# Optimization experiments

Hardware: AMD Instinct MI355X
Metric: run time of the kernel (lower is better)

The kernel has to match this reference:

```python
import jax, jax.numpy as jnp
import numpy as np

B, N, E, H = 64, 512, 1024, 16
DH = E // H


def setup_inputs() -> dict:
    key = jax.random.key(0)
    ks = jax.random.split(key, 5)
    x = jax.random.normal(ks[0], (B, N, E), dtype=jnp.float32)
    # Linear weights stored as [in, out] (transpose of torch's [out, in]); y = x @ W + b
    Wqkv = jax.random.normal(ks[1], (E, 3 * E), dtype=jnp.float32) * 0.02
    bqkv = jnp.zeros((3 * E,), dtype=jnp.float32)
    Wproj = jax.random.normal(ks[2], (E, E), dtype=jnp.float32) * 0.02
    bproj = jnp.zeros((E,), dtype=jnp.float32)
    adj = jax.random.randint(ks[3], (N, N), 0, 2, dtype=jnp.int32)
    return {"x": x, "Wqkv": Wqkv, "bqkv": bqkv, "Wproj": Wproj, "bproj": bproj, "adj": adj}


def reference(x, Wqkv, bqkv, Wproj, bproj, adj):
    b, n, e = x.shape
    h, dh = H, e // H
    # fused QKV projection
    qkv = (x @ Wqkv + bqkv).reshape(b, n, 3, h, dh)
    qkv = jnp.transpose(qkv, (2, 0, 3, 1, 4))  # [3, B, H, N, Dh]
    q, k, v = qkv[0], qkv[1], qkv[2]
    # adjacency mask with self-loops (adj + eye, then bool), broadcast over B, H
    mask = (adj + jnp.eye(n, dtype=adj.dtype)) > 0  # [N, N]
    scale = 1.0 / jnp.sqrt(jnp.asarray(dh, dtype=x.dtype))
    scores = jnp.einsum("bhnd,bhmd->bhnm", q, k) * scale  # [B, H, N, N]
    scores = jnp.where(mask[None, None], scores, jnp.finfo(scores.dtype).min)
    attn = jax.nn.softmax(scores, axis=-1)
    y = jnp.einsum("bhnm,bhmd->bhnd", attn, v)  # [B, H, N, Dh]
    y = jnp.transpose(y, (0, 2, 1, 3)).reshape(b, n, e)
    return y @ Wproj + bproj
```

## Files before the change

### kernel.cpp

```cpp
#include <hip/hip_runtime.h>
#include <hip/hip_bf16.h>

#define Bz 64
#define Nz 512
#define Ez 1024
#define Hz 16
#define DHz 64

static constexpr int MROWS = Bz * Nz;
static constexpr int NQKV  = 3 * Ez;

typedef __attribute__((ext_vector_type(8))) short bf16x8_t;
typedef __attribute__((ext_vector_type(4))) float f32x4_t;
typedef __attribute__((ext_vector_type(16))) float f32x16_t;
typedef __attribute__((ext_vector_type(4))) unsigned u32x4_t;

union FragU { bf16x8_t h; u32x4_t u; };

__device__ __forceinline__ unsigned short f2bf(float f) {
    union { float f; unsigned u; } v; v.f = f;
    unsigned r = v.u + 0x7FFFu + ((v.u >> 16) & 1u);
    return (unsigned short)(r >> 16);
}
__device__ __forceinline__ float bf2f(unsigned short h) {
    union { unsigned u; float f; } v; v.u = ((unsigned)h) << 16;
    return v.f;
}
__device__ __forceinline__ unsigned packbf(float a, float b) {
    union { float f; unsigned u; } x, y; x.f = a; y.f = b;
    return ((x.u + 0x8000u) >> 16) | ((y.u + 0x8000u) & 0xFFFF0000u);
}

__device__ __forceinline__ void async16(const unsigned short* g, unsigned short* l) {
    __builtin_amdgcn_global_load_lds(
        (const __attribute__((address_space(1))) void*)g,
        (__attribute__((address_space(3))) void*)l, 16, 0, 0);
}

__global__ void cvt_f32_bf16(const float* __restrict__ in,
                             unsigned short* __restrict__ out, int n4) {
    int id = blockIdx.x * blockDim.x + threadIdx.x;
    int stride = gridDim.x * blockDim.x;
    for (int i = id; i < n4; i += stride) {
        float4 f = ((const float4*)in)[i];
        ushort4 o;
        o.x = f2bf(f.x); o.y = f2bf(f.y); o.z = f2bf(f.z); o.w = f2bf(f.w);
        ((ushort4*)out)[i] = o;
    }
}

__global__ __launch_bounds__(256)
void cvt_transpose(const float* __restrict__ in,
                   unsigned short* __restrict__ out,
                   int K, int Ncols) {
    int n  = blockIdx.x * 256 + threadIdx.x;
    int k0 = blockIdx.y * 8;
    bf16x8_t o;
#pragma unroll
    for (int j = 0; j < 8; j++)
        o[j] = (short)f2bf(in[(long)(k0 + j) * Ncols + n]);
    *(bf16x8_t*)&out[(long)n * K + k0] = o;
}

__global__ void build_adjm(const int* __restrict__ adj,
                           unsigned long long* __restrict__ adjm) {
    int id = blockIdx.x * blockDim.x + threadIdx.x;
    int n = id >> 3, w = id & 7;
    const int4* r4 = (const int4*)(adj + (long)n * Nz + w * 64);
    unsigned long long m = 0;
#pragma unroll
    for (int c = 0; c < 16; c++) {
        int4 v = r4[c];
        unsigned long long bits =
            (unsigned long long)(v.x != 0) | ((unsigned long long)(v.y != 0) << 1) |
            ((unsigned long long)(v.z != 0) << 2) | ((unsigned long long)(v.w != 0) << 3);
        m |= bits << (c * 4);
    }
    if ((n >> 6) == w) m |= 1ull << (n & 63);
    adjm[id] = m;
}

template<bool OUT_BF16>
__global__ __launch_bounds__(256)
void gemm_mfma(const unsigned short* __restrict__ A,
               const unsigned short* __restrict__ BT,
               const float* __restrict__ bias,
               void* __restrict__ C,
               int M, int Ncols, int K) {
    const int tid  = threadIdx.x;
    const int wave = tid >> 6;
    const int lane = tid & 63;
    const int wm = (wave >> 1) * 64;
    const int wn = (wave & 1) * 64;
    const int m32 = lane & 31;
    const int kh  = lane >> 5;

    const int rowBase = blockIdx.y * 128;
    const int colBase = blockIdx.x * 128;

    __shared__ __align__(16) unsigned short As[128][64];
    __shared__ __align__(16) unsigned short Bs[128][64];

    f32x16_t acc[2][2];
#pragma unroll
    for (int i = 0; i < 2; i++)
#pragma unroll
        for (int j = 0; j < 2; j++)
#pragma unroll
            for (int r = 0; r < 16; r++)
                acc[i][j][r] = 0.0f;

    const unsigned short* pa[4];
    const unsigned short* pb[4];
#pragma unroll
    for (int cc = 0; cc < 4; cc++) {
        int s = tid + cc * 256;
        int r = s >> 3;
        int c = (s & 7) ^ (r & 7);
        pa[cc] = &A [(long)(rowBase + r) * K + c * 8];
        pb[cc] = &BT[(long)(colBase + r) * K + c * 8];
    }
    const int fsw = m32 & 7;

    for (int k0 = 0; k0 < K; k0 += 64) {
        __syncthreads();
#pragma unroll
        for (int cc = 0; cc < 4; cc++) {
            async16(pa[cc] + k0, (unsigned short*)As + (size_t)(cc * 64 + wave * 16) * 32);
            async16(pb[cc] + k0, (unsigned short*)Bs + (size_t)(cc * 64 + wave * 16) * 32);
        }
        __syncthreads();

        bf16x8_t af[2][4], bfr[2][4];
#pragma unroll
        for (int kc = 0; kc < 4; kc++) {
            int p = (kc * 2 + kh) ^ fsw;
#pragma unroll
            for (int t = 0; t < 2; t++) {
                af[t][kc]  = *(bf16x8_t*)&As[wm + t * 32 + m32][p * 8];
                bfr[t][kc] = *(bf16x8_t*)&Bs[wn + t * 32 + m32][p * 8];
            }
        }
#pragma unroll
        for (int kc = 0; kc < 4; kc++)
#pragma unroll
            for (int i = 0; i < 2; i++)
#pragma unroll
                for (int j = 0; j < 2; j++)
                    acc[i][j] = __builtin_amdgcn_mfma_f32_32x32x16_bf16(
                        af[i][kc], bfr[j][kc], acc[i][j], 0, 0, 0);
    }

#pragma unroll
    for (int j = 0; j < 2; j++) {
        int col = colBase + wn + j * 32 + m32;
        float bv = bias[col];
#pragma unroll
        for (int i = 0; i < 2; i++) {
#pragma unroll
            for (int reg = 0; reg < 16; reg++) {
                int row = rowBase + wm + i * 32 + (reg & 3) + 8 * (reg >> 2) + 4 * kh;
                float v = acc[i][j][reg] + bv;
                if (OUT_BF16)
                    ((unsigned short*)C)[(long)row * Ncols + col] = f2bf(v);
                else
                    ((float*)C)[(long)row * Ncols + col] = v;
            }
        }
    }
}

__global__ __launch_bounds__(512, 2)
void attn_mfma(const unsigned short* __restrict__ qkv,
               const unsigned long long* __restrict__ adjm,
               unsigned short* __restrict__ y)
{
    const int h = blockIdx.x;
    const int b = blockIdx.y;
    const int tid  = threadIdx.x;
    const int lane = tid & 63;
    const int w    = tid >> 6;
    const int l16  = lane & 15;
    const int q    = lane >> 4;

    __shared__ __align__(16) unsigned short Ks[512][64];
    __shared__ __align__(16) unsigned short Vt[64][512];

    const long rowB = (long)b * Nz;
    const unsigned short* base = qkv + rowB * NQKV;

    for (int idx = tid; idx < 4096; idx += 512) {
        int n = idx >> 3, cc = idx & 7;
        *(bf16x8_t*)&Ks[n][(cc ^ (n & 7)) * 8] =
            *(const bf16x8_t*)&base[(long)n * NQKV + Ez + h * DHz + cc * 8];
    }
    {
        int tp = tid & 255, dh = tid >> 8;
        int n0 = tp * 2;
        bf16x8_t va[4], vb[4];
#pragma unroll
        for (int c = 0; c < 4; c++) {
            va[c] = *(const bf16x8_t*)&base[(long)n0 * NQKV + 2 * Ez + h * DHz + dh * 32 + c * 8];
            vb[c] = *(const bf16x8_t*)&base[(long)(n0 + 1) * NQKV + 2 * Ez + h * DHz + dh * 32 + c * 8];
        }
        unsigned short* vt = &Vt[0][0];
#pragma unroll
        for (int dd = 0; dd < 32; dd++) {
            int d = dh * 32 + dd;
            unsigned lo = (unsigned)(unsigned short)va[dd >> 3][dd & 7];
            unsigned hi = (unsigned)(unsigned short)vb[dd >> 3][dd & 7];
            int cp = (n0 >> 3) ^ (d & 7);
            *(unsigned*)&vt[d * 512 + cp * 8 + (n0 & 7)] = lo | (hi << 16);
        }
    }
    FragU qf[4][2];
#pragma unroll
    for (int mt = 0; mt < 4; mt++)
#pragma unroll
        for (int kc = 0; kc < 2; kc++)
            qf[mt][kc].h = *(const bf16x8_t*)&base[(long)(w * 64 + mt * 16 + l16) * NQKV
                                                   + h * DHz + kc * 32 + q * 8];
    __syncthreads();

    f32x4_t oacc[4][4];
#pragma unroll
    for (int mt = 0; mt < 4; mt++)
#pragma unroll
        for (int dt = 0; dt < 4; dt++) {
            f32x4_t z = {0.0f, 0.0f, 0.0f, 0.0f};
            oacc[mt][dt] = z;
        }
    float rsum[4] = {0.0f, 0.0f, 0.0f, 0.0f};
    unsigned long long wm[4];

    for (int ct = 0; ct < 16; ct++) {
        const int j0 = ct * 32;
        if ((ct & 1) == 0) {
#pragma unroll
            for (int mt = 0; mt < 4; mt++)
                wm[mt] = adjm[(size_t)(w * 64 + mt * 16 + l16) * 8 + (ct >> 1)];
        }
        bf16x8_t kf[2][2];
#pragma unroll
        for (int jt = 0; jt < 2; jt++)
#pragma unroll
            for (int kc = 0; kc < 2; kc++)
                kf[jt][kc] = *(const bf16x8_t*)
                    &Ks[j0 + jt * 16 + l16][((kc * 4 + q) ^ (l16 & 7)) * 8];

        f32x4_t tacc[2][4];
#pragma unroll
        for (int jt = 0; jt < 2; jt++)
#pragma unroll
            for (int mt = 0; mt < 4; mt++) {
                f32x4_t z = {0.0f, 0.0f, 0.0f, 0.0f};
                z = __builtin_amdgcn_mfma_f32_16x16x32_bf16(kf[jt][0], qf[mt][0].h, z, 0, 0, 0);
                tacc[jt][mt] = __builtin_amdgcn_mfma_f32_16x16x32_bf16(kf[jt][1], qf[mt][1].h, z, 0, 0, 0);
            }

        unsigned pk[2][4][2];
#pragma unroll
        for (int jt = 0; jt < 2; jt++)
#pragma unroll
            for (int mt = 0; mt < 4; mt++) {
                float e[4];
#pragma unroll
                for (int r = 0; r < 4; r++) {
                    int jrel = (ct & 1) * 32 + jt * 16 + q * 4 + r;
                    bool bit = (wm[mt] >> jrel) & 1ull;
                    float ev = bit ? __expf(tacc[jt][mt][r] * 0.125f) : 0.0f;
                    e[r] = ev;
                    rsum[mt] += ev;
                }
                pk[jt][mt][0] = packbf(e[0], e[1]);
                pk[jt][mt][1] = packbf(e[2], e[3]);
            }

        bf16x8_t vf[4];
#pragma unroll
        for (int dt = 0; dt < 4; dt++) {
            int d = dt * 16 + l16;
            int cp = (ct * 4 + q) ^ (l16 & 7);
            vf[dt] = *(const bf16x8_t*)&(&Vt[0][0])[d * 512 + cp * 8];
        }

#pragma unroll
        for (int mt = 0; mt < 4; mt++) {
            FragU pf;
#pragma unroll
            for (int p = 0; p < 4; p++) {
                int srcl = ((lane & 16) << 1) | ((p & 2) << 3) | l16;
                unsigned a0 = (unsigned)__shfl((int)pk[0][mt][p & 1], srcl);
                unsigned a1 = (unsigned)__shfl((int)pk[1][mt][p & 1], srcl);
                pf.u[p] = (lane & 32) ? a1 : a0;
            }
#pragma unroll
            for (int dt = 0; dt < 4; dt++)
                oacc[mt][dt] = __builtin_amdgcn_mfma_f32_16x16x32_bf16(
                    pf.h, vf[dt], oacc[mt][dt], 0, 0, 0);
        }
    }

#pragma unroll
    for (int mt = 0; mt < 4; mt++) {
        float s = rsum[mt];
        s += __shfl_xor(s, 16);
        s += __shfl_xor(s, 32);
#pragma unroll
        for (int r = 0; r < 4; r++) {
            float rs = __shfl(s, (lane & 48) | (q * 4) | r);
            float inv = 1.0f / rs;
            int row = w * 64 + mt * 16 + q * 4 + r;
#pragma unroll
            for (int dt = 0; dt < 4; dt++)
                y[(rowB + row) * Ez + h * DHz + dt * 16 + l16] =
                    f2bf(oacc[mt][dt][r] * inv);
        }
    }
}

extern "C" void kernel_launch(void* const* d_in, const int* in_sizes, int n_in,
                              void* d_out, int out_size, void* d_ws, size_t ws_size,
                              hipStream_t stream) {
    const float* x     = (const float*)d_in[0];
    const float* Wqkv  = (const float*)d_in[1];
    const float* bqkv  = (const float*)d_in[2];
    const float* Wproj = (const float*)d_in[3];
    const float* bproj = (const float*)d_in[4];
    const int*   adj   = (const int*)d_in[5];
    float* out = (float*)d_out;

    char* ws = (char*)d_ws;
    unsigned short* xb     = (unsigned short*)(ws);
    unsigned short* qkv    = (unsigned short*)(ws + 67108864);
    unsigned short* WqkvT  = (unsigned short*)(ws + 268435456);
    unsigned short* WprojT = (unsigned short*)(ws + 274726912);
    unsigned long long* adjm = (unsigned long long*)(ws + 276824064);
    unsigned short* yb = xb;

    cvt_f32_bf16<<<8192, 256, 0, stream>>>(x, xb, (Bz * Nz * Ez) / 4);
    cvt_transpose<<<dim3(NQKV / 256, Ez / 8), 256, 0, stream>>>(Wqkv, WqkvT, Ez, NQKV);
    cvt_transpose<<<dim3(Ez / 256, Ez / 8), 256, 0, stream>>>(Wproj, WprojT, Ez, Ez);
    build_adjm<<<16, 256, 0, stream>>>(adj, adjm);

    gemm_mfma<true><<<dim3(NQKV / 128, MROWS / 128), 256, 0, stream>>>(
        xb, WqkvT, bqkv, qkv, MROWS, NQKV, Ez);

    attn_mfma<<<dim3(Hz, Bz), 512, 0, stream>>>(qkv, adjm, yb);

    gemm_mfma<false><<<dim3(Ez / 128, MROWS / 128), 256, 0, stream>>>(
        yb, WprojT, bproj, out, MROWS, Ez, Ez);
}
```

Baseline: 744.0 us.

## Restructure GEMM to 256x256 tiles with double-buffered async LDS pipeline

The bf16 MFMA GEMM goes from 128x128 tiles with 4 waves to 256x256 tiles with 8 waves. Global-to-LDS async loads for A and B are double-buffered and staggered across two half-phases per k-step, so loads overlap MFMA work and synchronisation is reduced. It also adds an XCD-aware block-index swizzle and raises wave priority around MFMA bursts. In exchange it uses four times the LDS (128KB) and more accumulator registers, which limits occupancy and adds fragile vmcnt-based synchronisation.

```diff
diff --git a/kernel.cpp b/kernel.cpp
--- a/kernel.cpp
+++ b/kernel.cpp
@@ -35,6 +35,13 @@
     __builtin_amdgcn_global_load_lds(
         (const __attribute__((address_space(1))) void*)g,
         (__attribute__((address_space(3))) void*)l, 16, 0, 0);
+}
+
+__device__ __forceinline__ void barrier_lds() {
+    asm volatile("s_waitcnt lgkmcnt(0)" ::: "memory");
+    __builtin_amdgcn_sched_barrier(0);
+    __builtin_amdgcn_s_barrier();
+    __builtin_amdgcn_sched_barrier(0);
 }
 
 __global__ void cvt_f32_bf16(const float* __restrict__ in,
@@ -81,90 +88,146 @@
 }
 
 template<bool OUT_BF16>
-__global__ __launch_bounds__(256)
+__global__ __launch_bounds__(512, 2)
 void gemm_mfma(const unsigned short* __restrict__ A,
                const unsigned short* __restrict__ BT,
                const float* __restrict__ bias,
                void* __restrict__ C,
                int M, int Ncols, int K) {
     const int tid  = threadIdx.x;
-    const int wave = tid >> 6;
+    const int w    = tid >> 6;
     const int lane = tid & 63;
-    const int wm = (wave >> 1) * 64;
-    const int wn = (wave & 1) * 64;
-    const int m32 = lane & 31;
-    const int kh  = lane >> 5;
-
-    const int rowBase = blockIdx.y * 128;
-    const int colBase = blockIdx.x * 128;
-
-    __shared__ __align__(16) unsigned short As[128][64];
-    __shared__ __align__(16) unsigned short Bs[128][64];
-
-    f32x16_t acc[2][2];
-#pragma unroll
-    for (int i = 0; i < 2; i++)
-#pragma unroll
-        for (int j = 0; j < 2; j++)
+    const int m32  = lane & 31;
+    const int kh   = lane >> 5;
+    const int wm   = (w >> 2) * 128;
+    const int wn   = (w & 3) * 64;
+
+    const int nwg = gridDim.x * gridDim.y;
+    const int bid = blockIdx.y * gridDim.x + blockIdx.x;
+    const int swz = (bid & 7) * (nwg >> 3) + (bid >> 3);
+    const int rowBase = (swz / gridDim.x) * 256;
+    const int colBase = (swz % gridDim.x) * 256;
+
+    __shared__ __align__(16) unsigned short Abuf[2][256][64];
+    __shared__ __align__(16) unsigned short Bbuf[2][256][64];
+
+    f32x16_t acc[4][2];
+#pragma unroll
+    for (int mi = 0; mi < 4; mi++)
+#pragma unroll
+        for (int n = 0; n < 2; n++)
 #pragma unroll
             for (int r = 0; r < 16; r++)
-                acc[i][j][r] = 0.0f;
-
-    const unsigned short* pa[4];
-    const unsigned short* pb[4];
-#pragma unroll
-    for (int cc = 0; cc < 4; cc++) {
-        int s = tid + cc * 256;
+                acc[mi][n][r] = 0.0f;
+
+    const unsigned short* srcA[4];
+    const unsigned short* srcB[4];
+#pragma unroll
+    for (int li = 0; li < 4; li++) {
+        int s = (w * 4 + li) * 64 + lane;
         int r = s >> 3;
         int c = (s & 7) ^ (r & 7);
-        pa[cc] = &A [(long)(rowBase + r) * K + c * 8];
-        pb[cc] = &BT[(long)(colBase + r) * K + c * 8];
-    }
+        srcA[li] = A  + (size_t)(rowBase + r) * K + c * 8;
+        srcB[li] = BT + (size_t)(colBase + r) * K + c * 8;
+    }
+    const int dstOff = w * 2048;
+
+    const int nt = K >> 6;
     const int fsw = m32 & 7;
 
-    for (int k0 = 0; k0 < K; k0 += 64) {
-        __syncthreads();
-#pragma unroll
-        for (int cc = 0; cc < 4; cc++) {
-            async16(pa[cc] + k0, (unsigned short*)As + (size_t)(cc * 64 + wave * 16) * 32);
-            async16(pb[cc] + k0, (unsigned short*)Bs + (size_t)(cc * 64 + wave * 16) * 32);
-        }
-        __syncthreads();
-
+#pragma unroll
+    for (int li = 0; li < 4; li++)
+        async16(srcA[li], (unsigned short*)Abuf[0] + dstOff + li * 512);
+#pragma unroll
+    for (int li = 0; li < 4; li++)
+        async16(srcB[li], (unsigned short*)Bbuf[0] + dstOff + li * 512);
+#pragma unroll
+    for (int li = 0; li < 4; li++)
+        async16(srcB[li] + 64, (unsigned short*)Bbuf[1] + dstOff + li * 512);
+    asm volatile("s_waitcnt vmcnt(4)" ::: "memory");
+    __builtin_amdgcn_sched_barrier(0);
+    __builtin_amdgcn_s_barrier();
+    __builtin_amdgcn_sched_barrier(0);
+
+    for (int t = 0; t < nt; t++) {
+        const int buf = t & 1;
         bf16x8_t af[2][4], bfr[2][4];
+
+        if (t + 1 < nt) {
+#pragma unroll
+            for (int li = 0; li < 4; li++)
+                async16(srcA[li] + (t + 1) * 64,
+                        (unsigned short*)Abuf[buf ^ 1] + dstOff + li * 512);
+        }
 #pragma unroll
         for (int kc = 0; kc < 4; kc++) {
             int p = (kc * 2 + kh) ^ fsw;
 #pragma unroll
-            for (int t = 0; t < 2; t++) {
-                af[t][kc]  = *(bf16x8_t*)&As[wm + t * 32 + m32][p * 8];
-                bfr[t][kc] = *(bf16x8_t*)&Bs[wn + t * 32 + m32][p * 8];
-            }
-        }
+            for (int n = 0; n < 2; n++)
+                bfr[n][kc] = *(const bf16x8_t*)&Bbuf[buf][wn + n * 32 + m32][p * 8];
+#pragma unroll
+            for (int mi = 0; mi < 2; mi++)
+                af[mi][kc] = *(const bf16x8_t*)&Abuf[buf][wm + mi * 32 + m32][p * 8];
+        }
+        __builtin_amdgcn_s_setprio(1);
 #pragma unroll
         for (int kc = 0; kc < 4; kc++)
 #pragma unroll
-            for (int i = 0; i < 2; i++)
-#pragma unroll
-                for (int j = 0; j < 2; j++)
-                    acc[i][j] = __builtin_amdgcn_mfma_f32_32x32x16_bf16(
-                        af[i][kc], bfr[j][kc], acc[i][j], 0, 0, 0);
-    }
-
-#pragma unroll
-    for (int j = 0; j < 2; j++) {
-        int col = colBase + wn + j * 32 + m32;
+            for (int mi = 0; mi < 2; mi++)
+#pragma unroll
+                for (int n = 0; n < 2; n++)
+                    acc[mi][n] = __builtin_amdgcn_mfma_f32_32x32x16_bf16(
+                        af[mi][kc], bfr[n][kc], acc[mi][n], 0, 0, 0);
+        __builtin_amdgcn_s_setprio(0);
+        barrier_lds();
+
+        if (t + 2 < nt) {
+#pragma unroll
+            for (int li = 0; li < 4; li++)
+                async16(srcB[li] + (t + 2) * 64,
+                        (unsigned short*)Bbuf[buf] + dstOff + li * 512);
+        }
+#pragma unroll
+        for (int kc = 0; kc < 4; kc++) {
+            int p = (kc * 2 + kh) ^ fsw;
+#pragma unroll
+            for (int mi = 0; mi < 2; mi++)
+                af[mi][kc] = *(const bf16x8_t*)&Abuf[buf][wm + 64 + mi * 32 + m32][p * 8];
+        }
+        __builtin_amdgcn_s_setprio(1);
+#pragma unroll
+        for (int kc = 0; kc < 4; kc++)
+#pragma unroll
+            for (int mi = 0; mi < 2; mi++)
+#pragma unroll
+                for (int n = 0; n < 2; n++)
+                    acc[2 + mi][n] = __builtin_amdgcn_mfma_f32_32x32x16_bf16(
+                        af[mi][kc], bfr[n][kc], acc[2 + mi][n], 0, 0, 0);
+        __builtin_amdgcn_s_setprio(0);
+
+        if (t + 2 < nt) {
+            asm volatile("s_waitcnt vmcnt(4)" ::: "memory");
+            barrier_lds();
+        } else if (t + 1 < nt) {
+            asm volatile("s_waitcnt vmcnt(0)" ::: "memory");
+            barrier_lds();
+        }
+    }
+
+#pragma unroll
+    for (int n = 0; n < 2; n++) {
+        int col = colBase + wn + n * 32 + m32;
         float bv = bias[col];
 #pragma unroll
-        for (int i = 0; i < 2; i++) {
+        for (int mi = 0; mi < 4; mi++) {
 #pragma unroll
             for (int reg = 0; reg < 16; reg++) {
-                int row = rowBase + wm + i * 32 + (reg & 3) + 8 * (reg >> 2) + 4 * kh;
-                float v = acc[i][j][reg] + bv;
+                int row = rowBase + wm + mi * 32 + (reg & 3) + 8 * (reg >> 2) + 4 * kh;
+                float v = acc[mi][n][reg] + bv;
                 if (OUT_BF16)
-                    ((unsigned short*)C)[(long)row * Ncols + col] = f2bf(v);
+                    ((unsigned short*)C)[(size_t)row * Ncols + col] = f2bf(v);
                 else
-                    ((float*)C)[(long)row * Ncols + col] = v;
+                    ((float*)C)[(size_t)row * Ncols + col] = v;
             }
         }
     }
@@ -343,11 +406,11 @@
     cvt_transpose<<<dim3(Ez / 256, Ez / 8), 256, 0, stream>>>(Wproj, WprojT, Ez, Ez);
     build_adjm<<<16, 256, 0, stream>>>(adj, adjm);
 
-    gemm_mfma<true><<<dim3(NQKV / 128, MROWS / 128), 256, 0, stream>>>(
+    gemm_mfma<true><<<dim3(NQKV / 256, MROWS / 256), 512, 0, stream>>>(
         xb, WqkvT, bqkv, qkv, MROWS, NQKV, Ez);
 
     attn_mfma<<<dim3(Hz, Bz), 512, 0, stream>>>(qkv, adjm, yb);
 
-    gemm_mfma<false><<<dim3(Ez / 128, MROWS / 128), 256, 0, stream>>>(
+    gemm_mfma<false><<<dim3(Ez / 256, MROWS / 256), 512, 0, stream>>>(
         yb, WprojT, bproj, out, MROWS, Ez, Ez);
 }
```

New measurement: 753.5 us. Within noise of the previous version (+1.3%).
